# Performance work log

Measured on AMD Instinct MI355X. Metric: run time of the kernel, lower is better.

## Reference

```python
import jax, jax.numpy as jnp
import numpy as np

N = 100000
E = 1600000
D_IN = 128
D_H = 128


def _sage_conv(x, src, dst, W_self, W_neigh, b, n_nodes):
    # mean aggregation over in-neighbors: dst receives from src
    gathered = x[src]                                        # [E, D]
    summed = jax.ops.segment_sum(gathered, dst, num_segments=n_nodes)  # [N, D]
    deg = jax.ops.segment_sum(jnp.ones((src.shape[0],), x.dtype), dst,
                              num_segments=n_nodes)          # [N]
    mean_neigh = summed / jnp.maximum(deg, 1.0)[:, None]     # zero-degree -> 0
    return x @ W_self + mean_neigh @ W_neigh + b


def setup_inputs() -> dict:
    key = jax.random.key(0)
    ks = jax.random.split(key, 9)
    s1 = 1.0 / np.sqrt(D_IN)
    s2 = 1.0 / np.sqrt(D_H)
    return {
        "in_feat": jax.random.normal(ks[0], (N, D_IN), jnp.float32),
        "W1_self": jax.random.uniform(ks[1], (D_IN, D_H), jnp.float32, -s1, s1),
        "W1_neigh": jax.random.uniform(ks[2], (D_IN, D_H), jnp.float32, -s1, s1),
        "b1": jnp.zeros((D_H,), jnp.float32),
        "W2_self": jax.random.uniform(ks[3], (D_H, D_H), jnp.float32, -s2, s2),
        "W2_neigh": jax.random.uniform(ks[4], (D_H, D_H), jnp.float32, -s2, s2),
        "b2": jnp.zeros((D_H,), jnp.float32),
        "src": jax.random.randint(ks[5], (E,), 0, N, jnp.int32),
        "dst": jax.random.randint(ks[6], (E,), 0, N, jnp.int32),
    }


def reference(in_feat, W1_self, W1_neigh, b1, W2_self, W2_neigh, b2, src, dst):
    h = _sage_conv(in_feat, src, dst, W1_self, W1_neigh, b1, N)
    h = jax.nn.relu(h)
    h = _sage_conv(h, src, dst, W2_self, W2_neigh, b2, N)
    return h
```

## Files before the change

kernel.cpp:

```cpp
#include <hip/hip_runtime.h>
#include <hip/hip_fp16.h>

#define D 128
#define NB_MAX 1024
#define PART_BLOCKS 512

using f32x4  = __attribute__((ext_vector_type(4))) float;
using half8  = __attribute__((ext_vector_type(8))) _Float16;
using short8 = __attribute__((ext_vector_type(8))) short;

#define AS1(p) ((const __attribute__((address_space(1))) void*)(p))
#define AS3(p) ((__attribute__((address_space(3))) void*)(p))

__global__ void convert_w_k(const float* __restrict__ Ws, const float* __restrict__ Wn,
                            unsigned short* __restrict__ Wg) {
    int idx = blockIdx.x * blockDim.x + threadIdx.x;
    if (idx >= 128 * 256) return;
    int col = idx >> 8;
    int k   = idx & 255;
    float v = (k < 128) ? Ws[k * D + col] : Wn[(k - 128) * D + col];
    _Float16 hv = (_Float16)v;
    _Float16 lv = (_Float16)(v - (float)hv);
    int kc = k >> 5, q = (k >> 3) & 3, j = k & 7;
    Wg[(((kc * 2 + 0) * 4 + q) * 128 + col) * 8 + j] = *(unsigned short*)&hv;
    Wg[(((kc * 2 + 1) * 4 + q) * 128 + col) * 8 + j] = *(unsigned short*)&lv;
}

__global__ void convert_x_k(const float* __restrict__ x, __half* __restrict__ y, int n4) {
    int i = blockIdx.x * blockDim.x + threadIdx.x;
    if (i < n4) {
        float4 v = *(const float4*)(x + (size_t)i * 4);
        __half2 h0 = __floats2half2_rn(v.x, v.y);
        __half2 h1 = __floats2half2_rn(v.z, v.w);
        __half2* o = (__half2*)(y + (size_t)i * 4);
        o[0] = h0; o[1] = h1;
    }
}

__global__ void zero_buckets_k(int* __restrict__ bucket_counts, int nb) {
    int i = blockIdx.x * blockDim.x + threadIdx.x;
    if (i < nb) bucket_counts[i] = 0;
}

__global__ void bucket_count_k(const int* __restrict__ dst, int* __restrict__ bucket_counts,
                               int E, int nb) {
    __shared__ int hist[NB_MAX];
    int t = threadIdx.x;
    for (int b = t; b < nb; b += 256) hist[b] = 0;
    __syncthreads();
    for (int i = blockIdx.x * 256 + t; i < E; i += gridDim.x * 256)
        atomicAdd(&hist[dst[i] >> 8], 1);
    __syncthreads();
    for (int b = t; b < nb; b += 256) {
        int c = hist[b];
        if (c) atomicAdd(&bucket_counts[b], c);
    }
}

__global__ void bucket_scan_k(const int* __restrict__ bucket_counts,
                              int* __restrict__ bucket_base,
                              int* __restrict__ bucket_cursor, int nb) {
    __shared__ int sh[256];
    int t = threadIdx.x;
    int base = t * 4;
    int v0 = (base + 0 < nb) ? bucket_counts[base + 0] : 0;
    int v1 = (base + 1 < nb) ? bucket_counts[base + 1] : 0;
    int v2 = (base + 2 < nb) ? bucket_counts[base + 2] : 0;
    int v3 = (base + 3 < nb) ? bucket_counts[base + 3] : 0;
    int tsum = v0 + v1 + v2 + v3;
    sh[t] = tsum;
    __syncthreads();
    for (int off = 1; off < 256; off <<= 1) {
        int x = 0;
        if (t >= off) x = sh[t - off];
        __syncthreads();
        if (t >= off) sh[t] += x;
        __syncthreads();
    }
    int excl = sh[t] - tsum;
    if (base + 0 < nb) { bucket_base[base+0] = excl;          bucket_cursor[base+0] = excl; }
    if (base + 1 < nb) { bucket_base[base+1] = excl+v0;       bucket_cursor[base+1] = excl+v0; }
    if (base + 2 < nb) { bucket_base[base+2] = excl+v0+v1;    bucket_cursor[base+2] = excl+v0+v1; }
    if (base + 3 < nb) { bucket_base[base+3] = excl+v0+v1+v2; bucket_cursor[base+3] = excl+v0+v1+v2; }
    if (t == 255) bucket_base[nb] = sh[255];
}

__global__ void partition_k(const int* __restrict__ src, const int* __restrict__ dst,
                            int* __restrict__ bucket_cursor, unsigned* __restrict__ pairs,
                            int E, int nb, int chunk) {
    __shared__ int hist[NB_MAX];
    __shared__ int bbase[NB_MAX];
    int t = threadIdx.x;
    int e0 = blockIdx.x * chunk;
    int e1 = min(E, e0 + chunk);
    for (int b = t; b < nb; b += 256) hist[b] = 0;
    __syncthreads();
    for (int i = e0 + t; i < e1; i += 256)
        atomicAdd(&hist[dst[i] >> 8], 1);
    __syncthreads();
    for (int b = t; b < nb; b += 256) {
        int c = hist[b];
        int bs = 0;
        if (c) bs = atomicAdd(&bucket_cursor[b], c);
        bbase[b] = bs;
        hist[b] = 0;
    }
    __syncthreads();
    for (int i = e0 + t; i < e1; i += 256) {
        int dd = dst[i];
        int b = dd >> 8;
        int r = atomicAdd(&hist[b], 1);
        pairs[bbase[b] + r] = ((unsigned)(dd & 255) << 17) | (unsigned)src[i];
    }
}

__global__ void build_csr_k(const unsigned* __restrict__ pairs,
                            const int* __restrict__ bucket_base,
                            int* __restrict__ counts, int* __restrict__ offsets,
                            int* __restrict__ edge_src, int N) {
    __shared__ int hist[256];
    __shared__ int curs[256];
    __shared__ int sh[256];
    int t = threadIdx.x;
    int b = blockIdx.x;
    int n0 = b << 8;
    int e0 = bucket_base[b];
    int e1 = bucket_base[b + 1];
    hist[t] = 0;
    __syncthreads();
    for (int i = e0 + t; i < e1; i += 256)
        atomicAdd(&hist[pairs[i] >> 17], 1);
    __syncthreads();
    int c = hist[t];
    sh[t] = c;
    __syncthreads();
    for (int off = 1; off < 256; off <<= 1) {
        int x = 0;
        if (t >= off) x = sh[t - off];
        __syncthreads();
        if (t >= off) sh[t] += x;
        __syncthreads();
    }
    int excl = sh[t] - c;
    curs[t] = excl;
    int node = n0 + t;
    if (node < N) { counts[node] = c; offsets[node] = e0 + excl; }
    __syncthreads();
    for (int i = e0 + t; i < e1; i += 256) {
        unsigned p = pairs[i];
        int pos = atomicAdd(&curs[p >> 17], 1);
        edge_src[e0 + pos] = (int)(p & 0x1FFFFu);
    }
}

__global__ void aggregate_f16_k(const __half* __restrict__ x,
                                const int* __restrict__ edge_src,
                                const int* __restrict__ offsets,
                                const int* __restrict__ counts,
                                __half* __restrict__ agg, int n) {
    int wid  = (blockIdx.x * blockDim.x + threadIdx.x) >> 6;
    int lane = threadIdx.x & 63;
    if (wid >= n) return;
    int sg  = lane >> 4;
    int sub = lane & 15;
    int start = offsets[wid];
    int cnt   = counts[wid];
    float acc[8] = {0.f, 0.f, 0.f, 0.f, 0.f, 0.f, 0.f, 0.f};
    for (int base = 0; base < cnt; base += 64) {
        int valid = min(64, cnt - base);
        int s = (lane < valid) ? edge_src[start + base + lane] : 0;
        int iter = (valid + 3) >> 2;
        #pragma unroll 2
        for (int k = 0; k < iter; ++k) {
            int idx = 4 * k + sg;
            int row = __shfl(s, idx);
            float wgt = (idx < valid) ? 1.0f : 0.0f;
            float4 raw = *(const float4*)(x + (size_t)row * D + sub * 8);
            const __half2* hp = (const __half2*)&raw;
            #pragma unroll
            for (int j = 0; j < 4; ++j) {
                float2 f = __half22float2(hp[j]);
                acc[2 * j]     = fmaf(f.x, wgt, acc[2 * j]);
                acc[2 * j + 1] = fmaf(f.y, wgt, acc[2 * j + 1]);
            }
        }
    }
    #pragma unroll
    for (int j = 0; j < 8; ++j) {
        acc[j] += __shfl(acc[j], lane ^ 16);
        acc[j] += __shfl(acc[j], lane ^ 32);
    }
    if (sg == 0) {
        float inv = 1.0f / fmaxf((float)cnt, 1.0f);
        union { __half2 h2[4]; short8 s8; } u;
        #pragma unroll
        for (int j = 0; j < 4; ++j)
            u.h2[j] = __floats2half2_rn(acc[2 * j] * inv, acc[2 * j + 1] * inv);
        *(short8*)(agg + (size_t)wid * D + sub * 8) = u.s8;
    }
}

__global__ __launch_bounds__(256)
void mfma_gemm_k(const _Float16* __restrict__ A0, const _Float16* __restrict__ A1,
                 const unsigned short* __restrict__ Wg,
                 const float* __restrict__ bias,
                 float* __restrict__ C, __half* __restrict__ Ch,
                 int n, int out_mode) {
    __shared__ __align__(16) unsigned short lds_b[8192];
    int t = threadIdx.x;
    int w = t >> 6;
    int l = t & 63;
    int m = l & 15;
    int q = l >> 4;
    int r0 = blockIdx.x * 128 + w * 32;

    f32x4 acc[2][8];
    #pragma unroll
    for (int rt = 0; rt < 2; ++rt)
        #pragma unroll
        for (int ct = 0; ct < 8; ++ct)
            acc[rt][ct] = (f32x4){0.f, 0.f, 0.f, 0.f};

    for (int kc = 0; kc < 8; ++kc) {
        const unsigned short* gk = Wg + (size_t)kc * 8192;
        #pragma unroll
        for (int i = 0; i < 4; ++i) {
            int e = i * 256 + t;
            __builtin_amdgcn_global_load_lds(AS1(gk + e * 8), AS3(lds_b + e * 8), 16, 0, 0);
        }
        const _Float16* __restrict__ A = (kc < 4) ? A0 : A1;
        int ka = (kc & 3) * 32;
        half8 a[2];
        #pragma unroll
        for (int rt = 0; rt < 2; ++rt) {
            int row = r0 + rt * 16 + m;
            half8 v = (half8){0, 0, 0, 0, 0, 0, 0, 0};
            if (row < n) v = *(const half8*)(A + (size_t)row * D + ka + q * 8);
            a[rt] = v;
        }
        __syncthreads();

        #pragma unroll
        for (int ct = 0; ct < 8; ++ct) {
            half8 bh = *(const half8*)&lds_b[(size_t)(q * 128 + ct * 16 + m) * 8];
            half8 bl = *(const half8*)&lds_b[(size_t)((4 + q) * 128 + ct * 16 + m) * 8];
            #pragma unroll
            for (int rt = 0; rt < 2; ++rt) {
                acc[rt][ct] = __builtin_amdgcn_mfma_f32_16x16x32_f16(a[rt], bh, acc[rt][ct], 0, 0, 0);
                acc[rt][ct] = __builtin_amdgcn_mfma_f32_16x16x32_f16(a[rt], bl, acc[rt][ct], 0, 0, 0);
            }
        }
        __syncthreads();
    }

    #pragma unroll
    for (int ct = 0; ct < 8; ++ct) {
        int col = ct * 16 + m;
        float bb = bias[col];
        #pragma unroll
        for (int rt = 0; rt < 2; ++rt) {
            #pragma unroll
            for (int r = 0; r < 4; ++r) {
                int row = r0 + rt * 16 + q * 4 + r;
                if (row < n) {
                    float v = acc[rt][ct][r] + bb;
                    if (out_mode) {
                        v = fmaxf(v, 0.f);
                        Ch[(size_t)row * D + col] = __float2half(v);
                    } else {
                        C[(size_t)row * D + col] = v;
                    }
                }
            }
        }
    }
}

extern "C" void kernel_launch(void* const* d_in, const int* in_sizes, int n_in,
                              void* d_out, int out_size, void* d_ws, size_t ws_size,
                              hipStream_t stream) {
    const float* in_feat = (const float*)d_in[0];
    const float* W1s     = (const float*)d_in[1];
    const float* W1n     = (const float*)d_in[2];
    const float* b1      = (const float*)d_in[3];
    const float* W2s     = (const float*)d_in[4];
    const float* W2n     = (const float*)d_in[5];
    const float* b2      = (const float*)d_in[6];
    const int*   src     = (const int*)d_in[7];
    const int*   dst     = (const int*)d_in[8];

    const int N  = in_sizes[0] / D;
    const int E  = in_sizes[7];
    const int NB = (N + 255) >> 8;

    char* base = (char*)d_ws;
    size_t off = 0;
    __half* agg16 = (__half*)(base + off); off += (size_t)N * D * 2;
    __half* xh16  = (__half*)(base + off); off += (size_t)N * D * 2;
    int* edge_src = (int*)(base + off);    off += (size_t)E * 4;
    int* counts   = (int*)(base + off);    off += (size_t)N * 4;
    int* offsets  = (int*)(base + off);    off += (size_t)N * 4;
    unsigned short* Wg1 = (unsigned short*)(base + off); off += 65536 * 2;
    unsigned short* Wg2 = (unsigned short*)(base + off); off += 65536 * 2;
    int* bucket_counts = (int*)(base + off); off += NB_MAX * 4;
    int* bucket_base   = (int*)(base + off); off += (NB_MAX + 1) * 4;
    off = (off + 15) & ~(size_t)15;
    int* bucket_cursor = (int*)(base + off); off += NB_MAX * 4;

    unsigned* pairs = (unsigned*)agg16;

    const int chunk = (E + PART_BLOCKS - 1) / PART_BLOCKS;

    hipLaunchKernelGGL(convert_w_k, dim3(128), dim3(256), 0, stream, W1s, W1n, Wg1);
    hipLaunchKernelGGL(convert_w_k, dim3(128), dim3(256), 0, stream, W2s, W2n, Wg2);
    {
        int n4 = (N * D) / 4;
        hipLaunchKernelGGL(convert_x_k, dim3((n4 + 255) / 256), dim3(256), 0, stream,
                           in_feat, xh16, n4);
    }

    hipLaunchKernelGGL(zero_buckets_k, dim3((NB + 255) / 256), dim3(256), 0, stream,
                       bucket_counts, NB);
    hipLaunchKernelGGL(bucket_count_k, dim3(PART_BLOCKS), dim3(256), 0, stream,
                       dst, bucket_counts, E, NB);
    hipLaunchKernelGGL(bucket_scan_k, dim3(1), dim3(256), 0, stream,
                       bucket_counts, bucket_base, bucket_cursor, NB);
    hipLaunchKernelGGL(partition_k, dim3(PART_BLOCKS), dim3(256), 0, stream,
                       src, dst, bucket_cursor, pairs, E, NB, chunk);
    hipLaunchKernelGGL(build_csr_k, dim3(NB), dim3(256), 0, stream,
                       pairs, bucket_base, counts, offsets, edge_src, N);

    const dim3 aggGrid(((size_t)N * 64 + 255) / 256);
    const dim3 gemmGrid((N + 127) / 128);

    hipLaunchKernelGGL(aggregate_f16_k, aggGrid, dim3(256), 0, stream,
                       xh16, edge_src, offsets, counts, agg16, N);
    hipLaunchKernelGGL(mfma_gemm_k, gemmGrid, dim3(256), 0, stream,
                       (const _Float16*)xh16, (const _Float16*)agg16, Wg1, b1,
                       (float*)nullptr, xh16, N, 1);

    hipLaunchKernelGGL(aggregate_f16_k, aggGrid, dim3(256), 0, stream,
                       xh16, edge_src, offsets, counts, agg16, N);
    hipLaunchKernelGGL(mfma_gemm_k, gemmGrid, dim3(256), 0, stream,
                       (const _Float16*)xh16, (const _Float16*)agg16, Wg2, b2,
                       (float*)d_out, (__half*)nullptr, N, 0);
}
```

Before: 391.0 us.

## Merge prep kernels, batch aggregation gathers, and widen GEMM blocks to 512 threads

Folds the weight conversion, feature conversion and bucket zeroing into one prep launch to cut launch overhead. In the aggregation kernel, four neighbour-row loads are now issued before any are accumulated, so more memory requests are in flight per wave. The GEMM block grows to 512 threads covering 256 rows, so each staged weight tile in LDS is shared by twice as many rows. The larger GEMM blocks may reduce occupancy or leave a partial tail block.

```diff
diff --git a/kernel.cpp b/kernel.cpp
--- a/kernel.cpp
+++ b/kernel.cpp
@@ -12,33 +12,44 @@
 #define AS1(p) ((const __attribute__((address_space(1))) void*)(p))
 #define AS3(p) ((__attribute__((address_space(3))) void*)(p))
 
-__global__ void convert_w_k(const float* __restrict__ Ws, const float* __restrict__ Wn,
-                            unsigned short* __restrict__ Wg) {
-    int idx = blockIdx.x * blockDim.x + threadIdx.x;
-    if (idx >= 128 * 256) return;
-    int col = idx >> 8;
-    int k   = idx & 255;
-    float v = (k < 128) ? Ws[k * D + col] : Wn[(k - 128) * D + col];
-    _Float16 hv = (_Float16)v;
-    _Float16 lv = (_Float16)(v - (float)hv);
-    int kc = k >> 5, q = (k >> 3) & 3, j = k & 7;
-    Wg[(((kc * 2 + 0) * 4 + q) * 128 + col) * 8 + j] = *(unsigned short*)&hv;
-    Wg[(((kc * 2 + 1) * 4 + q) * 128 + col) * 8 + j] = *(unsigned short*)&lv;
-}
-
-__global__ void convert_x_k(const float* __restrict__ x, __half* __restrict__ y, int n4) {
-    int i = blockIdx.x * blockDim.x + threadIdx.x;
-    if (i < n4) {
-        float4 v = *(const float4*)(x + (size_t)i * 4);
-        __half2 h0 = __floats2half2_rn(v.x, v.y);
-        __half2 h1 = __floats2half2_rn(v.z, v.w);
-        __half2* o = (__half2*)(y + (size_t)i * 4);
-        o[0] = h0; o[1] = h1;
-    }
-}
-
-__global__ void zero_buckets_k(int* __restrict__ bucket_counts, int nb) {
-    int i = blockIdx.x * blockDim.x + threadIdx.x;
+__global__ void prep_k(const float* __restrict__ x, __half* __restrict__ y, int n4,
+                       const float* __restrict__ W1s, const float* __restrict__ W1n,
+                       const float* __restrict__ W2s, const float* __restrict__ W2n,
+                       unsigned short* __restrict__ Wg1, unsigned short* __restrict__ Wg2,
+                       int* __restrict__ bucket_counts, int nb, int xb) {
+    int b = blockIdx.x;
+    int t = threadIdx.x;
+    if (b < xb) {
+        int i = b * 256 + t;
+        if (i < n4) {
+            float4 v = *(const float4*)(x + (size_t)i * 4);
+            __half2 h0 = __floats2half2_rn(v.x, v.y);
+            __half2 h1 = __floats2half2_rn(v.z, v.w);
+            __half2* o = (__half2*)(y + (size_t)i * 4);
+            o[0] = h0; o[1] = h1;
+        }
+        return;
+    }
+    int wb = b - xb;
+    if (wb < 512) {
+        int sel = wb >> 8;
+        int lb  = wb & 255;
+        if (lb >= 128) return;
+        const float* Ws = sel ? W2s : W1s;
+        const float* Wn = sel ? W2n : W1n;
+        unsigned short* Wg = sel ? Wg2 : Wg1;
+        int idx = lb * 256 + t;
+        int col = idx >> 8;
+        int k   = idx & 255;
+        float v = (k < 128) ? Ws[k * D + col] : Wn[(k - 128) * D + col];
+        _Float16 hv = (_Float16)v;
+        _Float16 lv = (_Float16)(v - (float)hv);
+        int kc = k >> 5, q = (k >> 3) & 3, j = k & 7;
+        Wg[(((kc * 2 + 0) * 4 + q) * 128 + col) * 8 + j] = *(unsigned short*)&hv;
+        Wg[(((kc * 2 + 1) * 4 + q) * 128 + col) * 8 + j] = *(unsigned short*)&lv;
+        return;
+    }
+    int i = (wb - 512) * 256 + t;
     if (i < nb) bucket_counts[i] = 0;
 }
 
@@ -169,19 +180,25 @@
     for (int base = 0; base < cnt; base += 64) {
         int valid = min(64, cnt - base);
         int s = (lane < valid) ? edge_src[start + base + lane] : 0;
-        int iter = (valid + 3) >> 2;
-        #pragma unroll 2
-        for (int k = 0; k < iter; ++k) {
-            int idx = 4 * k + sg;
-            int row = __shfl(s, idx);
-            float wgt = (idx < valid) ? 1.0f : 0.0f;
-            float4 raw = *(const float4*)(x + (size_t)row * D + sub * 8);
-            const __half2* hp = (const __half2*)&raw;
+        for (int k0 = 0; k0 < valid; k0 += 16) {
+            float4 raw[4];
+            float  wg[4];
             #pragma unroll
-            for (int j = 0; j < 4; ++j) {
-                float2 f = __half22float2(hp[j]);
-                acc[2 * j]     = fmaf(f.x, wgt, acc[2 * j]);
-                acc[2 * j + 1] = fmaf(f.y, wgt, acc[2 * j + 1]);
+            for (int u = 0; u < 4; ++u) {
+                int idx = k0 + 4 * u + sg;
+                int row = __shfl(s, idx & 63);
+                wg[u] = (idx < valid) ? 1.0f : 0.0f;
+                raw[u] = *(const float4*)(x + (size_t)row * D + sub * 8);
+            }
+            #pragma unroll
+            for (int u = 0; u < 4; ++u) {
+                const __half2* hp = (const __half2*)&raw[u];
+                #pragma unroll
+                for (int j = 0; j < 4; ++j) {
+                    float2 f = __half22float2(hp[j]);
+                    acc[2 * j]     = fmaf(f.x, wg[u], acc[2 * j]);
+                    acc[2 * j + 1] = fmaf(f.y, wg[u], acc[2 * j + 1]);
+                }
             }
         }
     }
@@ -200,7 +217,7 @@
     }
 }
 
-__global__ __launch_bounds__(256)
+__global__ __launch_bounds__(512)
 void mfma_gemm_k(const _Float16* __restrict__ A0, const _Float16* __restrict__ A1,
                  const unsigned short* __restrict__ Wg,
                  const float* __restrict__ bias,
@@ -212,7 +229,7 @@
     int l = t & 63;
     int m = l & 15;
     int q = l >> 4;
-    int r0 = blockIdx.x * 128 + w * 32;
+    int r0 = blockIdx.x * 256 + w * 32;
 
     f32x4 acc[2][8];
     #pragma unroll
@@ -224,8 +241,8 @@
     for (int kc = 0; kc < 8; ++kc) {
         const unsigned short* gk = Wg + (size_t)kc * 8192;
         #pragma unroll
-        for (int i = 0; i < 4; ++i) {
-            int e = i * 256 + t;
+        for (int i = 0; i < 2; ++i) {
+            int e = i * 512 + t;
             __builtin_amdgcn_global_load_lds(AS1(gk + e * 8), AS3(lds_b + e * 8), 16, 0, 0);
         }
         const _Float16* __restrict__ A = (kc < 4) ? A0 : A1;
@@ -310,17 +327,14 @@
     unsigned* pairs = (unsigned*)agg16;
 
     const int chunk = (E + PART_BLOCKS - 1) / PART_BLOCKS;
-
-    hipLaunchKernelGGL(convert_w_k, dim3(128), dim3(256), 0, stream, W1s, W1n, Wg1);
-    hipLaunchKernelGGL(convert_w_k, dim3(128), dim3(256), 0, stream, W2s, W2n, Wg2);
-    {
-        int n4 = (N * D) / 4;
-        hipLaunchKernelGGL(convert_x_k, dim3((n4 + 255) / 256), dim3(256), 0, stream,
-                           in_feat, xh16, n4);
-    }
-
-    hipLaunchKernelGGL(zero_buckets_k, dim3((NB + 255) / 256), dim3(256), 0, stream,
-                       bucket_counts, NB);
+    const int n4 = (N * D) / 4;
+    const int xb = (n4 + 255) / 256;
+    const int zb = (NB + 255) / 256;
+
+    hipLaunchKernelGGL(prep_k, dim3(xb + 512 + zb), dim3(256), 0, stream,
+                       in_feat, xh16, n4, W1s, W1n, W2s, W2n, Wg1, Wg2,
+                       bucket_counts, NB, xb);
+
     hipLaunchKernelGGL(bucket_count_k, dim3(PART_BLOCKS), dim3(256), 0, stream,
                        dst, bucket_counts, E, NB);
     hipLaunchKernelGGL(bucket_scan_k, dim3(1), dim3(256), 0, stream,
@@ -331,17 +345,17 @@
                        pairs, bucket_base, counts, offsets, edge_src, N);
 
     const dim3 aggGrid(((size_t)N * 64 + 255) / 256);
-    const dim3 gemmGrid((N + 127) / 128);
+    const dim3 gemmGrid((N + 255) / 256);
 
     hipLaunchKernelGGL(aggregate_f16_k, aggGrid, dim3(256), 0, stream,
                        xh16, edge_src, offsets, counts, agg16, N);
-    hipLaunchKernelGGL(mfma_gemm_k, gemmGrid, dim3(256), 0, stream,
+    hipLaunchKernelGGL(mfma_gemm_k, gemmGrid, dim3(512), 0, stream,
                        (const _Float16*)xh16, (const _Float16*)agg16, Wg1, b1,
                        (float*)nullptr, xh16, N, 1);
 
     hipLaunchKernelGGL(aggregate_f16_k, aggGrid, dim3(256), 0, stream,
                        xh16, edge_src, offsets, counts, agg16, N);
-    hipLaunchKernelGGL(mfma_gemm_k, gemmGrid, dim3(256), 0, stream,
+    hipLaunchKernelGGL(mfma_gemm_k, gemmGrid, dim3(512), 0, stream,
                        (const _Float16*)xh16, (const _Float16*)agg16, Wg2, b2,
                        (float*)d_out, (__half*)nullptr, N, 0);
 }
```

New measurement: 352.4 us. 9.9% less time.
